# Optimization experiments

Measured on AMD Instinct MI355X. Metric: run time of the kernel, lower is better.

## Reference

```python
import jax, jax.numpy as jnp
import numpy as np

SYM_LIST = np.array([0, 2, 5], dtype=np.int64)


def quat_to_rot_wxyz(q):
    """q: [bs, 4] normalized quaternion in wxyz order -> [bs, 3, 3] rotation."""
    w, x, y, z = q[:, 0], q[:, 1], q[:, 2], q[:, 3]
    two = jnp.asarray(2.0, q.dtype)
    one = jnp.asarray(1.0, q.dtype)
    r00 = one - two * (y * y + z * z)
    r01 = two * (x * y - z * w)
    r02 = two * (x * z + y * w)
    r10 = two * (x * y + z * w)
    r11 = one - two * (x * x + z * z)
    r12 = two * (y * z - x * w)
    r20 = two * (x * z - y * w)
    r21 = two * (y * z + x * w)
    r22 = one - two * (x * x + y * y)
    R = jnp.stack([
        jnp.stack([r00, r01, r02], axis=-1),
        jnp.stack([r10, r11, r12], axis=-1),
        jnp.stack([r20, r21, r22], axis=-1),
    ], axis=-2)  # [bs, 3, 3]
    return R


def setup_inputs() -> dict:
    key = jax.random.key(0)
    k1, k2, k3, k4, k5 = jax.random.split(key, 5)
    bs, num_p = 32, 2048
    pred_r = jax.random.normal(k1, (bs, 4), dtype=jnp.float32)
    pred_t = jax.random.normal(k2, (bs, 3), dtype=jnp.float32)
    target = jax.random.normal(k3, (bs, num_p, 3), dtype=jnp.float32)
    model_points = jax.random.normal(k4, (bs, num_p, 3), dtype=jnp.float32)
    idx = jax.random.randint(k5, (bs, 1), 0, 8, dtype=jnp.int64)
    return {"pred_r": pred_r, "pred_t": pred_t, "target": target,
            "model_points": model_points, "idx": idx, "permutation": 0}


def reference(pred_r, pred_t, target, model_points, idx, permutation):
    # normalize quaternion, build rotation, transform model points (row-vector
    # convention as in torch.bmm(model_points, base))
    q = pred_r / jnp.linalg.norm(pred_r, axis=1, keepdims=True)  # [bs,4]
    R = quat_to_rot_wxyz(q)                                      # [bs,3,3]
    tf = jnp.einsum('bnd,bde->bne', model_points, R) + pred_t[:, None, :]  # [bs,N,3]

    # brute-force 1-NN: for each transformed model point, nearest target point
    # squared distances via the ||a||^2 + ||b||^2 - 2 a.b expansion: [bs,N,N]
    d2 = (jnp.sum(tf * tf, axis=-1)[:, :, None]
          + jnp.sum(target * target, axis=-1)[:, None, :]
          - 2.0 * jnp.einsum('bnd,bmd->bnm', tf, target))
    inds = jnp.argmin(d2, axis=-1)                               # [bs,N]
    matched = jnp.take_along_axis(target, inds[..., None], axis=1)  # [bs,N,3]

    # apply the symmetric (ADD-S) matching only for classes in sym_list
    sym_mask = jnp.isin(idx[:, 0], jnp.asarray(SYM_LIST))        # [bs]
    target2 = jnp.where(sym_mask[:, None, None], matched, target)

    dis = jnp.mean(jnp.linalg.norm(tf - target, axis=2), axis=1)    # ADD (returned)
    dis2 = jnp.mean(jnp.linalg.norm(tf - target2, axis=2), axis=1)  # ADD-S (knn-matched)
    return jnp.stack([dis, dis2])  # [2, bs]
```

## Files before the change

kernel.cpp:

```cpp
#include <hip/hip_runtime.h>
#include <math.h>

#define NP      2048
#define BS      32
#define TPB     512
#define NW      (TPB / 64)
#define MSLICE  (NP / NW)
#define PPT     4
#define PTSBLK  (64 * PPT)
#define SLICES  (NP / PTSBLK)

__global__ void zero_out_kernel(float* __restrict__ out) {
    int i = threadIdx.x;
    if (i < 64) out[i] = 0.0f;
}

__global__ __launch_bounds__(TPB) void loss_kernel(
    const float* __restrict__ pred_r,
    const float* __restrict__ pred_t,
    const float* __restrict__ target,
    const float* __restrict__ model_points,
    const int*   __restrict__ idx,
    float* __restrict__ out)
{
    __shared__ float4 tgt[NP];
    __shared__ float4 ptf[PTSBLK];
    __shared__ float  pe[NW][PTSBLK];
    __shared__ int    pm[NW][PTSBLK];
    __shared__ float  red1[NW], red2[NW];

    const int b    = blockIdx.x >> 3;
    const int s    = blockIdx.x & 7;
    const int tid  = threadIdx.x;
    const int wave = tid >> 6;
    const int lane = tid & 63;

    float qw = pred_r[b * 4 + 0];
    float qx = pred_r[b * 4 + 1];
    float qy = pred_r[b * 4 + 2];
    float qz = pred_r[b * 4 + 3];
    float nrm = sqrtf(qw * qw + qx * qx + qy * qy + qz * qz);
    qw /= nrm; qx /= nrm; qy /= nrm; qz /= nrm;

    const float r00 = 1.0f - 2.0f * (qy * qy + qz * qz);
    const float r01 = 2.0f * (qx * qy - qz * qw);
    const float r02 = 2.0f * (qx * qz + qy * qw);
    const float r10 = 2.0f * (qx * qy + qz * qw);
    const float r11 = 1.0f - 2.0f * (qx * qx + qz * qz);
    const float r12 = 2.0f * (qy * qz - qx * qw);
    const float r20 = 2.0f * (qx * qz - qy * qw);
    const float r21 = 2.0f * (qy * qz + qx * qw);
    const float r22 = 1.0f - 2.0f * (qx * qx + qy * qy);

    const float tx = pred_t[b * 3 + 0];
    const float ty = pred_t[b * 3 + 1];
    const float tz = pred_t[b * 3 + 2];

    const float* tb = target + (size_t)b * NP * 3;
    #pragma unroll
    for (int k = 0; k < NP / TPB; ++k) {
        int j = tid + k * TPB;
        float t0 = tb[j * 3 + 0];
        float t1 = tb[j * 3 + 1];
        float t2 = tb[j * 3 + 2];
        tgt[j] = make_float4(t0, t1, t2, (t0 * t0 + t1 * t1) + t2 * t2);
    }

    float ax[PPT], ay[PPT], az[PPT], eb[PPT];
    int   mb[PPT];
    const float* mpb = model_points + (size_t)b * NP * 3;
    #pragma unroll
    for (int p = 0; p < PPT; ++p) {
        int n = s * PTSBLK + p * 64 + lane;
        float m0 = mpb[n * 3 + 0], m1 = mpb[n * 3 + 1], m2 = mpb[n * 3 + 2];
        float tfx = m0 * r00 + m1 * r10 + m2 * r20 + tx;
        float tfy = m0 * r01 + m1 * r11 + m2 * r21 + ty;
        float tfz = m0 * r02 + m1 * r12 + m2 * r22 + tz;
        ax[p] = -2.0f * tfx; ay[p] = -2.0f * tfy; az[p] = -2.0f * tfz;
        eb[p] = INFINITY;    mb[p] = 0;
        if (wave == 0) ptf[p * 64 + lane] = make_float4(tfx, tfy, tfz, 0.0f);
    }
    __syncthreads();

    const int mbase = wave * MSLICE;
    #pragma unroll 2
    for (int mm = 0; mm < MSLICE; mm += 4) {
        float4 c0 = tgt[mbase + mm + 0];
        float4 c1 = tgt[mbase + mm + 1];
        float4 c2 = tgt[mbase + mm + 2];
        float4 c3 = tgt[mbase + mm + 3];
        #pragma unroll
        for (int p = 0; p < PPT; ++p) {
            float e0 = fmaf(ax[p], c0.x, fmaf(ay[p], c0.y, fmaf(az[p], c0.z, c0.w)));
            if (e0 < eb[p]) { eb[p] = e0; mb[p] = mbase + mm + 0; }
            float e1 = fmaf(ax[p], c1.x, fmaf(ay[p], c1.y, fmaf(az[p], c1.z, c1.w)));
            if (e1 < eb[p]) { eb[p] = e1; mb[p] = mbase + mm + 1; }
            float e2 = fmaf(ax[p], c2.x, fmaf(ay[p], c2.y, fmaf(az[p], c2.z, c2.w)));
            if (e2 < eb[p]) { eb[p] = e2; mb[p] = mbase + mm + 2; }
            float e3 = fmaf(ax[p], c3.x, fmaf(ay[p], c3.y, fmaf(az[p], c3.z, c3.w)));
            if (e3 < eb[p]) { eb[p] = e3; mb[p] = mbase + mm + 3; }
        }
    }

    #pragma unroll
    for (int p = 0; p < PPT; ++p) {
        pe[wave][p * 64 + lane] = eb[p];
        pm[wave][p * 64 + lane] = mb[p];
    }
    __syncthreads();

    float s1 = 0.0f, s2 = 0.0f;
    if (tid < PTSBLK) {
        float bestE = pe[0][tid];
        int   bestM = pm[0][tid];
        #pragma unroll
        for (int w = 1; w < NW; ++w) {
            float e = pe[w][tid];
            int   m = pm[w][tid];
            if (e < bestE) { bestE = e; bestM = m; }
        }
        int n = s * PTSBLK + tid;
        float4 tf = ptf[tid];
        float4 tn = tgt[n];
        float dx = tf.x - tn.x, dy = tf.y - tn.y, dz = tf.z - tn.z;
        float dis = sqrtf(dx * dx + dy * dy + dz * dz);
        float dis2 = dis;
        int iv = idx[b];
        bool sym = (iv == 0) | (iv == 2) | (iv == 5);
        if (sym) {
            float4 tm = tgt[bestM];
            float sx = tf.x - tm.x, sy = tf.y - tm.y, sz = tf.z - tm.z;
            dis2 = sqrtf(sx * sx + sy * sy + sz * sz);
        }
        s1 = dis; s2 = dis2;
    }

    #pragma unroll
    for (int off = 32; off > 0; off >>= 1) {
        s1 += __shfl_down(s1, off);
        s2 += __shfl_down(s2, off);
    }
    if (lane == 0) { red1[wave] = s1; red2[wave] = s2; }
    __syncthreads();
    if (tid == 0) {
        float t1 = 0.0f, t2 = 0.0f;
        #pragma unroll
        for (int w = 0; w < NW; ++w) { t1 += red1[w]; t2 += red2[w]; }
        atomicAdd(out + b,      t1 * (1.0f / NP));
        atomicAdd(out + 32 + b, t2 * (1.0f / NP));
    }
}

extern "C" void kernel_launch(void* const* d_in, const int* in_sizes, int n_in,
                              void* d_out, int out_size, void* d_ws, size_t ws_size,
                              hipStream_t stream) {
    const float* pred_r       = (const float*)d_in[0];
    const float* pred_t       = (const float*)d_in[1];
    const float* target       = (const float*)d_in[2];
    const float* model_points = (const float*)d_in[3];
    const int*   idx          = (const int*)d_in[4];
    float* out = (float*)d_out;

    zero_out_kernel<<<1, 64, 0, stream>>>(out);
    loss_kernel<<<BS * SLICES, TPB, 0, stream>>>(pred_r, pred_t, target,
                                                 model_points, idx, out);
}
```

Baseline: 87.15 us.

## Split NN argmin over target quarters with workspace partials and a finish kernel

The 1-NN search is split so each block handles one quarter of the target points, with 8 points per thread, and writes per-point partial minima and indices to workspace. A second kernel merges the four partials, computes the ADD and ADD-S distances and reduces them with atomics. Output zeroing moves into the first kernel, which removes the separate zero launch. This aims for a smaller LDS footprint, more register-level reuse of each target load and more blocks, at the cost of a second launch and a global round trip. Because the zeroing sits in block 0 of the first kernel, it depends on kernel ordering on the stream before the finish kernel's atomics.

```diff
diff --git a/kernel.cpp b/kernel.cpp
--- a/kernel.cpp
+++ b/kernel.cpp
@@ -1,39 +1,39 @@
 #include <hip/hip_runtime.h>
 #include <math.h>
 
-#define NP      2048
-#define BS      32
-#define TPB     512
-#define NW      (TPB / 64)
-#define MSLICE  (NP / NW)
-#define PPT     4
-#define PTSBLK  (64 * PPT)
-#define SLICES  (NP / PTSBLK)
-
-__global__ void zero_out_kernel(float* __restrict__ out) {
-    int i = threadIdx.x;
-    if (i < 64) out[i] = 0.0f;
-}
-
-__global__ __launch_bounds__(TPB) void loss_kernel(
+#define NP        2048
+#define BS        32
+#define TPB       512
+#define NW        (TPB / 64)
+#define QUARTERS  4
+#define QSIZE     (NP / QUARTERS)
+#define WSLICE    (QSIZE / NW)
+#define PPT       8
+#define PTSBLK    (64 * PPT)
+#define PSLICES   (NP / PTSBLK)
+
+__global__ __launch_bounds__(TPB) void argmin_part_kernel(
     const float* __restrict__ pred_r,
     const float* __restrict__ pred_t,
     const float* __restrict__ target,
     const float* __restrict__ model_points,
-    const int*   __restrict__ idx,
+    float* __restrict__ we,
+    int*   __restrict__ wm,
     float* __restrict__ out)
 {
-    __shared__ float4 tgt[NP];
-    __shared__ float4 ptf[PTSBLK];
+    __shared__ float4 tgt[QSIZE];
     __shared__ float  pe[NW][PTSBLK];
     __shared__ int    pm[NW][PTSBLK];
-    __shared__ float  red1[NW], red2[NW];
-
-    const int b    = blockIdx.x >> 3;
-    const int s    = blockIdx.x & 7;
+
+    const int bid  = blockIdx.x;
+    const int b    = bid >> 4;
+    const int q    = (bid >> 2) & 3;
+    const int s    = bid & 3;
     const int tid  = threadIdx.x;
     const int wave = tid >> 6;
     const int lane = tid & 63;
+
+    if (bid == 0 && tid < 64) out[tid] = 0.0f;
 
     float qw = pred_r[b * 4 + 0];
     float qx = pred_r[b * 4 + 1];
@@ -56,14 +56,11 @@
     const float ty = pred_t[b * 3 + 1];
     const float tz = pred_t[b * 3 + 2];
 
-    const float* tb = target + (size_t)b * NP * 3;
-    #pragma unroll
-    for (int k = 0; k < NP / TPB; ++k) {
-        int j = tid + k * TPB;
-        float t0 = tb[j * 3 + 0];
-        float t1 = tb[j * 3 + 1];
-        float t2 = tb[j * 3 + 2];
-        tgt[j] = make_float4(t0, t1, t2, (t0 * t0 + t1 * t1) + t2 * t2);
+    {
+        int g = q * QSIZE + tid;
+        const float* tp = target + ((size_t)b * NP + g) * 3;
+        float t0 = tp[0], t1 = tp[1], t2 = tp[2];
+        tgt[tid] = make_float4(t0, t1, t2, (t0 * t0 + t1 * t1) + t2 * t2);
     }
 
     float ax[PPT], ay[PPT], az[PPT], eb[PPT];
@@ -77,28 +74,28 @@
         float tfy = m0 * r01 + m1 * r11 + m2 * r21 + ty;
         float tfz = m0 * r02 + m1 * r12 + m2 * r22 + tz;
         ax[p] = -2.0f * tfx; ay[p] = -2.0f * tfy; az[p] = -2.0f * tfz;
-        eb[p] = INFINITY;    mb[p] = 0;
-        if (wave == 0) ptf[p * 64 + lane] = make_float4(tfx, tfy, tfz, 0.0f);
+        eb[p] = INFINITY;    mb[p] = q * QSIZE;
     }
     __syncthreads();
 
-    const int mbase = wave * MSLICE;
+    const int lc = wave * WSLICE;
     #pragma unroll 2
-    for (int mm = 0; mm < MSLICE; mm += 4) {
-        float4 c0 = tgt[mbase + mm + 0];
-        float4 c1 = tgt[mbase + mm + 1];
-        float4 c2 = tgt[mbase + mm + 2];
-        float4 c3 = tgt[mbase + mm + 3];
+    for (int mm = 0; mm < WSLICE; mm += 4) {
+        float4 c0 = tgt[lc + mm + 0];
+        float4 c1 = tgt[lc + mm + 1];
+        float4 c2 = tgt[lc + mm + 2];
+        float4 c3 = tgt[lc + mm + 3];
+        const int gm = q * QSIZE + lc + mm;
         #pragma unroll
         for (int p = 0; p < PPT; ++p) {
             float e0 = fmaf(ax[p], c0.x, fmaf(ay[p], c0.y, fmaf(az[p], c0.z, c0.w)));
-            if (e0 < eb[p]) { eb[p] = e0; mb[p] = mbase + mm + 0; }
+            if (e0 < eb[p]) { eb[p] = e0; mb[p] = gm + 0; }
             float e1 = fmaf(ax[p], c1.x, fmaf(ay[p], c1.y, fmaf(az[p], c1.z, c1.w)));
-            if (e1 < eb[p]) { eb[p] = e1; mb[p] = mbase + mm + 1; }
+            if (e1 < eb[p]) { eb[p] = e1; mb[p] = gm + 1; }
             float e2 = fmaf(ax[p], c2.x, fmaf(ay[p], c2.y, fmaf(az[p], c2.z, c2.w)));
-            if (e2 < eb[p]) { eb[p] = e2; mb[p] = mbase + mm + 2; }
+            if (e2 < eb[p]) { eb[p] = e2; mb[p] = gm + 2; }
             float e3 = fmaf(ax[p], c3.x, fmaf(ay[p], c3.y, fmaf(az[p], c3.z, c3.w)));
-            if (e3 < eb[p]) { eb[p] = e3; mb[p] = mbase + mm + 3; }
+            if (e3 < eb[p]) { eb[p] = e3; mb[p] = gm + 3; }
         }
     }
 
@@ -109,32 +106,91 @@
     }
     __syncthreads();
 
-    float s1 = 0.0f, s2 = 0.0f;
-    if (tid < PTSBLK) {
+    {
         float bestE = pe[0][tid];
         int   bestM = pm[0][tid];
         #pragma unroll
         for (int w = 1; w < NW; ++w) {
             float e = pe[w][tid];
-            int   m = pm[w][tid];
-            if (e < bestE) { bestE = e; bestM = m; }
+            if (e < bestE) { bestE = e; bestM = pm[w][tid]; }
         }
-        int n = s * PTSBLK + tid;
-        float4 tf = ptf[tid];
-        float4 tn = tgt[n];
-        float dx = tf.x - tn.x, dy = tf.y - tn.y, dz = tf.z - tn.z;
-        float dis = sqrtf(dx * dx + dy * dy + dz * dz);
-        float dis2 = dis;
-        int iv = idx[b];
-        bool sym = (iv == 0) | (iv == 2) | (iv == 5);
-        if (sym) {
-            float4 tm = tgt[bestM];
-            float sx = tf.x - tm.x, sy = tf.y - tm.y, sz = tf.z - tm.z;
-            dis2 = sqrtf(sx * sx + sy * sy + sz * sz);
-        }
-        s1 = dis; s2 = dis2;
-    }
-
+        size_t o = ((size_t)q * BS + b) * NP + (size_t)s * PTSBLK + tid;
+        we[o] = bestE;
+        wm[o] = bestM;
+    }
+}
+
+#define TPB2 256
+__global__ __launch_bounds__(TPB2) void finish_kernel(
+    const float* __restrict__ pred_r,
+    const float* __restrict__ pred_t,
+    const float* __restrict__ target,
+    const float* __restrict__ model_points,
+    const int*   __restrict__ idx,
+    const float* __restrict__ we,
+    const int*   __restrict__ wm,
+    float* __restrict__ out)
+{
+    __shared__ float red1[TPB2 / 64], red2[TPB2 / 64];
+
+    const int b    = blockIdx.x >> 3;
+    const int s    = blockIdx.x & 7;
+    const int tid  = threadIdx.x;
+    const int wave = tid >> 6;
+    const int lane = tid & 63;
+    const int n    = s * TPB2 + tid;
+
+    float qw = pred_r[b * 4 + 0];
+    float qx = pred_r[b * 4 + 1];
+    float qy = pred_r[b * 4 + 2];
+    float qz = pred_r[b * 4 + 3];
+    float nrm = sqrtf(qw * qw + qx * qx + qy * qy + qz * qz);
+    qw /= nrm; qx /= nrm; qy /= nrm; qz /= nrm;
+
+    const float r00 = 1.0f - 2.0f * (qy * qy + qz * qz);
+    const float r01 = 2.0f * (qx * qy - qz * qw);
+    const float r02 = 2.0f * (qx * qz + qy * qw);
+    const float r10 = 2.0f * (qx * qy + qz * qw);
+    const float r11 = 1.0f - 2.0f * (qx * qx + qz * qz);
+    const float r12 = 2.0f * (qy * qz - qx * qw);
+    const float r20 = 2.0f * (qx * qz - qy * qw);
+    const float r21 = 2.0f * (qy * qz + qx * qw);
+    const float r22 = 1.0f - 2.0f * (qx * qx + qy * qy);
+
+    const float tx = pred_t[b * 3 + 0];
+    const float ty = pred_t[b * 3 + 1];
+    const float tz = pred_t[b * 3 + 2];
+
+    size_t o0 = (size_t)b * NP + n;
+    float bestE = we[o0];
+    int   bestM = wm[o0];
+    #pragma unroll
+    for (int q = 1; q < QUARTERS; ++q) {
+        size_t o = ((size_t)q * BS + b) * NP + n;
+        float e = we[o];
+        if (e < bestE) { bestE = e; bestM = wm[o]; }
+    }
+
+    const float* mpp = model_points + ((size_t)b * NP + n) * 3;
+    float m0 = mpp[0], m1 = mpp[1], m2 = mpp[2];
+    float tfx = m0 * r00 + m1 * r10 + m2 * r20 + tx;
+    float tfy = m0 * r01 + m1 * r11 + m2 * r21 + ty;
+    float tfz = m0 * r02 + m1 * r12 + m2 * r22 + tz;
+
+    const float* tn = target + ((size_t)b * NP + n) * 3;
+    float dx = tfx - tn[0], dy = tfy - tn[1], dz = tfz - tn[2];
+    float dis = sqrtf(dx * dx + dy * dy + dz * dz);
+    float dis2 = dis;
+
+    int iv = idx[b];
+    bool sym = (iv == 0) | (iv == 2) | (iv == 5);
+    if (sym) {
+        const float* tm = target + ((size_t)b * NP + bestM) * 3;
+        float sx = tfx - tm[0], sy = tfy - tm[1], sz = tfz - tm[2];
+        dis2 = sqrtf(sx * sx + sy * sy + sz * sz);
+    }
+
+    float s1 = dis, s2 = dis2;
     #pragma unroll
     for (int off = 32; off > 0; off >>= 1) {
         s1 += __shfl_down(s1, off);
@@ -143,9 +199,8 @@
     if (lane == 0) { red1[wave] = s1; red2[wave] = s2; }
     __syncthreads();
     if (tid == 0) {
-        float t1 = 0.0f, t2 = 0.0f;
-        #pragma unroll
-        for (int w = 0; w < NW; ++w) { t1 += red1[w]; t2 += red2[w]; }
+        float t1 = (red1[0] + red1[1]) + (red1[2] + red1[3]);
+        float t2 = (red2[0] + red2[1]) + (red2[2] + red2[3]);
         atomicAdd(out + b,      t1 * (1.0f / NP));
         atomicAdd(out + 32 + b, t2 * (1.0f / NP));
     }
@@ -161,7 +216,11 @@
     const int*   idx          = (const int*)d_in[4];
     float* out = (float*)d_out;
 
-    zero_out_kernel<<<1, 64, 0, stream>>>(out);
-    loss_kernel<<<BS * SLICES, TPB, 0, stream>>>(pred_r, pred_t, target,
-                                                 model_points, idx, out);
+    float* we = (float*)d_ws;
+    int*   wm = (int*)((char*)d_ws + (size_t)QUARTERS * BS * NP * sizeof(float));
+
+    argmin_part_kernel<<<BS * QUARTERS * PSLICES, TPB, 0, stream>>>(
+        pred_r, pred_t, target, model_points, we, wm, out);
+    finish_kernel<<<BS * 8, TPB2, 0, stream>>>(
+        pred_r, pred_t, target, model_points, idx, we, wm, out);
 }
```

New measurement: 85.50 us. About the same (-1.9%).
